# Kernel optimization log

Measured on AMD Instinct MI355X. Metric: run time of the kernel, lower is better.

The kernel has to match this reference:

```python
import jax, jax.numpy as jnp
import numpy as np

N_NODES = 10000
N_EDGES = 320000
DIM = 256
NUM_HEADS = 8
HEAD_DIM = DIM // NUM_HEADS


def setup_inputs() -> dict:
    key = jax.random.key(0)
    ks = jax.random.split(key, 8)
    s = 1.0 / np.sqrt(DIM)
    x = jax.random.normal(ks[0], (N_NODES, DIM), dtype=jnp.float32)
    src = jax.random.randint(ks[1], (N_EDGES,), 0, N_NODES, dtype=jnp.int32)
    dst = jax.random.randint(ks[2], (N_EDGES,), 0, N_NODES, dtype=jnp.int32)
    Wq = jax.random.normal(ks[3], (DIM, DIM), dtype=jnp.float32) * s
    Wk = jax.random.normal(ks[4], (DIM, DIM), dtype=jnp.float32) * s
    Wv = jax.random.normal(ks[5], (DIM, DIM), dtype=jnp.float32) * s
    Wo = jax.random.normal(ks[6], (DIM, DIM), dtype=jnp.float32) * s
    z = jnp.zeros((DIM,), dtype=jnp.float32)
    return {"x": x, "src": src, "dst": dst,
            "Wq": Wq, "bq": z, "Wk": Wk, "bk": z,
            "Wv": Wv, "bv": z, "Wo": Wo, "bo": z}


def reference(x, src, dst, Wq, bq, Wk, bk, Wv, bv, Wo, bo):
    N = x.shape[0]
    # nn.Linear: y = x @ W.T + b
    q = (x @ Wq.T + bq).reshape(N, NUM_HEADS, HEAD_DIM)
    k = (x @ Wk.T + bk).reshape(N, NUM_HEADS, HEAD_DIM)
    v = (x @ Wv.T + bv).reshape(N, NUM_HEADS, HEAD_DIM)
    # u_dot_v: dot(q[src], k[dst]) per head -> [E, H]
    score = jnp.einsum('ehd,ehd->eh', q[src], k[dst]) / np.sqrt(HEAD_DIM).astype(np.float32)
    # Faithful to source: F.softmax(dim=1) on [E, H, 1] -> softmax over HEADS axis
    attn = jax.nn.softmax(score, axis=1)  # [E, H]
    # u_mul_e then sum-reduce onto destination nodes
    m = v[src] * attn[:, :, None]  # [E, H, HEAD_DIM]
    h = jax.ops.segment_sum(m, dst, num_segments=N).reshape(N, DIM)
    out = h @ Wo.T + bo
    # dropout p=0.0 -> identity
    return out
```

## Files before the change

### kernel.cpp

```cpp
#include <hip/hip_runtime.h>
#include <stdint.h>

#define N_NODES 10000
#define N_EDGES 320000
#define DIM 256
#define NRANGE 4
#define RANGE_DIV 2500
#define PAD_SLOTS 32

typedef _Float16 half8 __attribute__((ext_vector_type(8)));
typedef _Float16 half2t __attribute__((ext_vector_type(2)));
typedef float floatx4 __attribute__((ext_vector_type(4)));

#define QK_SCALE 0.17677669529663687f

typedef __attribute__((address_space(3))) uint32_t lds_u32;
typedef __attribute__((address_space(1))) const uint32_t glob_u32;
__device__ __forceinline__ void load16_lds(const _Float16* g, _Float16* l) {
  __builtin_amdgcn_global_load_lds((glob_u32*)g, (lds_u32*)l, 16, 0, 0);
}

__device__ __forceinline__ half8 cvt8s(const float4 a, const float4 b, float sc) {
  half8 o;
  o[0] = (_Float16)(a.x * sc); o[1] = (_Float16)(a.y * sc);
  o[2] = (_Float16)(a.z * sc); o[3] = (_Float16)(a.w * sc);
  o[4] = (_Float16)(b.x * sc); o[5] = (_Float16)(b.y * sc);
  o[6] = (_Float16)(b.z * sc); o[7] = (_Float16)(b.w * sc);
  return o;
}

__global__ void __launch_bounds__(256) prep_k(
    const float* __restrict__ x, const float* __restrict__ Wq,
    const float* __restrict__ Wk, const float* __restrict__ Wv,
    const float* __restrict__ Wo,
    _Float16* __restrict__ xh, _Float16* __restrict__ Wcat,
    _Float16* __restrict__ Woh) {
  int b = blockIdx.x;
  int t = threadIdx.x;
  if (b < 1250) {
    int i = b * 256 + t;
    const float4* p = (const float4*)x;
    ((half8*)xh)[i] = cvt8s(p[2 * i], p[2 * i + 1], 1.0f);
  } else {
    int bb = b - 1250;
    int w = bb >> 5;
    int i = (bb & 31) * 256 + t;
    const float* in = (w == 0) ? Wq : (w == 1) ? Wv : (w == 2) ? Wk : Wo;
    _Float16* out = (w < 3) ? (Wcat + (size_t)w * 65536) : Woh;
    float sc = (w == 0) ? QK_SCALE : 1.0f;
    const float4* p = (const float4*)in;
    ((half8*)out)[i] = cvt8s(p[2 * i], p[2 * i + 1], sc);
  }
}

template <int MODE>
__global__ void __launch_bounds__(256) gemm_tiled(
    const _Float16* __restrict__ A, const _Float16* __restrict__ B,
    const float* __restrict__ b0, const float* __restrict__ b1,
    const float* __restrict__ b2,
    _Float16* __restrict__ qv, _Float16* __restrict__ kh,
    float* __restrict__ outf, int M) {
  __shared__ _Float16 As[8192];
  __shared__ _Float16 Bs[8192];
  int t = threadIdx.x;
  int lane = t & 63;
  int wid = t >> 6;
  int l16 = lane & 15;
  int quad = lane >> 4;
  int wm = wid >> 1, wn = wid & 1;
  int m0 = blockIdx.x * 128;
  int n0 = blockIdx.y * 128;

  floatx4 acc[4][4];
#pragma unroll
  for (int i = 0; i < 4; ++i)
#pragma unroll
    for (int j = 0; j < 4; ++j) acc[i][j] = (floatx4){0.f, 0.f, 0.f, 0.f};

  for (int ks = 0; ks < 4; ++ks) {
    if (ks) __syncthreads();
#pragma unroll
    for (int i = 0; i < 4; ++i) {
      int idx = i * 4 + wid;
      int c = idx >> 1;
      int h = idx & 1;
      int r = h * 64 + lane;
      int ar = m0 + r;
      if (ar >= M) ar = M - 1;
      load16_lds(A + (size_t)ar * 256 + ks * 64 + c * 8, &As[(c * 128 + h * 64) * 8]);
      load16_lds(B + (size_t)(n0 + r) * 256 + ks * 64 + c * 8, &Bs[(c * 128 + h * 64) * 8]);
    }
    __syncthreads();
#pragma unroll
    for (int kk = 0; kk < 2; ++kk) {
      int j = kk * 4 + quad;
      half8 af[4], bf[4];
#pragma unroll
      for (int i = 0; i < 4; ++i) {
        af[i] = *(const half8*)&As[(j * 128 + wm * 64 + i * 16 + l16) * 8];
        bf[i] = *(const half8*)&Bs[(j * 128 + wn * 64 + i * 16 + l16) * 8];
      }
#pragma unroll
      for (int mi = 0; mi < 4; ++mi)
#pragma unroll
        for (int ni = 0; ni < 4; ++ni)
          acc[mi][ni] =
              __builtin_amdgcn_mfma_f32_16x16x32_f16(af[mi], bf[ni], acc[mi][ni], 0, 0, 0);
    }
  }

#pragma unroll
  for (int mi = 0; mi < 4; ++mi) {
#pragma unroll
    for (int ni = 0; ni < 4; ++ni) {
      int col = n0 + wn * 64 + ni * 16 + l16;
      float bias;
      if (MODE == 0) {
        bias = (col < 256) ? b0[col] * QK_SCALE
                           : (col < 512) ? b1[col - 256] : b2[col - 512];
      } else {
        bias = b0[col];
      }
#pragma unroll
      for (int r = 0; r < 4; ++r) {
        int row = m0 + wm * 64 + mi * 16 + quad * 4 + r;
        if (row < M) {
          float val = acc[mi][ni][r] + bias;
          if (MODE == 0) {
            if (col < 512)
              qv[(size_t)row * 512 + col] = (_Float16)val;
            else
              kh[(size_t)row * 256 + (col - 512)] = (_Float16)val;
          } else {
            outf[(size_t)row * 256 + col] = val;
          }
        }
      }
    }
  }
}

__global__ void scatter_k(const int* __restrict__ dst, const int* __restrict__ src,
                          int* __restrict__ cnt4, int* __restrict__ slist4) {
  int e = blockIdx.x * blockDim.x + threadIdx.x;
  if (e < N_EDGES) {
    int s = src[e];
    int r = s / RANGE_DIV;
    int cell = dst[e] * NRANGE + r;
    int pos = atomicAdd(&cnt4[cell], 1);
    if (pos < PAD_SLOTS) slist4[cell * PAD_SLOTS + pos] = s;
  }
}

__global__ void __launch_bounds__(256) aggregate_k(
    const _Float16* __restrict__ qv, const _Float16* __restrict__ kh,
    const int* __restrict__ slist4, const int* __restrict__ cnt4,
    _Float16* __restrict__ hh) {
  int lane = threadIdx.x & 63;
  int n = blockIdx.x * 4 + (threadIdx.x >> 6);
  if (n >= N_NODES) return;
  int h = lane & 7;
  int g = lane >> 3;

  half8 kc[4];
  const half8* krow = (const half8*)(kh + (size_t)n * DIM + h * 32);
#pragma unroll
  for (int i = 0; i < 4; ++i) kc[i] = krow[i];
  const half2t* k2 = (const half2t*)kc;

  half2t acc[16];
#pragma unroll
  for (int i = 0; i < 16; ++i) acc[i] = (half2t){(_Float16)0.f, (_Float16)0.f};

#pragma unroll 1
  for (int r = 0; r < NRANGE; ++r) {
    int cell = n * NRANGE + r;
    int deg = cnt4[cell];
    if (deg > PAD_SLOTS) deg = PAD_SLOTS;
    if (deg == 0) continue;
    const int* base = slist4 + (size_t)cell * PAD_SLOTS;
    int sid = 0;
    if (lane < deg) sid = base[lane];
    int iters = (deg + 7) >> 3;

    int idx = g;
    int s = __shfl(sid, idx);
    const half8* rr = (const half8*)(qv + (size_t)s * 512 + h * 32);
    half8 qc[4], vc[4];
#pragma unroll
    for (int i = 0; i < 4; ++i) { qc[i] = rr[i]; vc[i] = rr[32 + i]; }
    bool valid = idx < deg;

    for (int jj = 0; jj < iters; ++jj) {
      half8 nq[4], nv[4];
      bool nvalid = false;
      if (jj + 1 < iters) {
        int nidx = (jj + 1) * 8 + g;
        int ns = __shfl(sid, nidx);
        const half8* nr = (const half8*)(qv + (size_t)ns * 512 + h * 32);
#pragma unroll
        for (int i = 0; i < 4; ++i) { nq[i] = nr[i]; nv[i] = nr[32 + i]; }
        nvalid = nidx < deg;
      }
      const half2t* q2 = (const half2t*)qc;
      float pa = 0.f, pb = 0.f, pc = 0.f, pd = 0.f;
#pragma unroll
      for (int i = 0; i < 4; ++i) {
#if __has_builtin(__builtin_amdgcn_fdot2)
        pa = __builtin_amdgcn_fdot2(q2[i], k2[i], pa, false);
        pb = __builtin_amdgcn_fdot2(q2[4 + i], k2[4 + i], pb, false);
        pc = __builtin_amdgcn_fdot2(q2[8 + i], k2[8 + i], pc, false);
        pd = __builtin_amdgcn_fdot2(q2[12 + i], k2[12 + i], pd, false);
#else
        pa += (float)q2[i][0] * (float)k2[i][0] + (float)q2[i][1] * (float)k2[i][1];
        pb += (float)q2[4 + i][0] * (float)k2[4 + i][0] + (float)q2[4 + i][1] * (float)k2[4 + i][1];
        pc += (float)q2[8 + i][0] * (float)k2[8 + i][0] + (float)q2[8 + i][1] * (float)k2[8 + i][1];
        pd += (float)q2[12 + i][0] * (float)k2[12 + i][0] + (float)q2[12 + i][1] * (float)k2[12 + i][1];
#endif
      }
      float p = (pa + pb) + (pc + pd);
      float ex = __expf(p);
      float ssum = ex;
      ssum += __shfl_xor(ssum, 1);
      ssum += __shfl_xor(ssum, 2);
      ssum += __shfl_xor(ssum, 4);
      float a = valid ? (ex * __frcp_rn(ssum)) : 0.f;
      _Float16 ah = (_Float16)a;
      half2t ah2 = (half2t){ah, ah};
      const half2t* v2 = (const half2t*)vc;
#pragma unroll
      for (int i = 0; i < 16; ++i) acc[i] += v2[i] * ah2;
#pragma unroll
      for (int i = 0; i < 4; ++i) { qc[i] = nq[i]; vc[i] = nv[i]; }
      valid = nvalid;
    }
  }

#pragma unroll
  for (int i = 0; i < 16; ++i) {
    union { half2t h2; int v; } u;
    u.h2 = acc[i]; u.v = __shfl_xor(u.v, 8);  acc[i] += u.h2;
    u.h2 = acc[i]; u.v = __shfl_xor(u.v, 16); acc[i] += u.h2;
    u.h2 = acc[i]; u.v = __shfl_xor(u.v, 32); acc[i] += u.h2;
  }
  if (g == 0) {
    half8* hrow = (half8*)(hh + (size_t)n * DIM + h * 32);
    const half8* a8 = (const half8*)acc;
#pragma unroll
    for (int i = 0; i < 4; ++i) hrow[i] = a8[i];
  }
}

extern "C" void kernel_launch(void* const* d_in, const int* in_sizes, int n_in,
                              void* d_out, int out_size, void* d_ws, size_t ws_size,
                              hipStream_t stream) {
  const float* x = (const float*)d_in[0];
  const int* src = (const int*)d_in[1];
  const int* dst = (const int*)d_in[2];
  const float* Wq = (const float*)d_in[3];
  const float* bq = (const float*)d_in[4];
  const float* Wk = (const float*)d_in[5];
  const float* bk = (const float*)d_in[6];
  const float* Wv = (const float*)d_in[7];
  const float* bv = (const float*)d_in[8];
  const float* Wo = (const float*)d_in[9];
  const float* bo = (const float*)d_in[10];

  char* p = (char*)d_ws;
  const size_t SZ_NODE_H = (size_t)N_NODES * DIM * sizeof(_Float16);
  _Float16* xh = (_Float16*)p; p += SZ_NODE_H;
  _Float16* qvv = (_Float16*)p; p += 2 * SZ_NODE_H;
  _Float16* kh = (_Float16*)p; p += SZ_NODE_H;
  _Float16* hh = (_Float16*)p; p += SZ_NODE_H;
  _Float16* Wcat = (_Float16*)p; p += (size_t)768 * 256 * sizeof(_Float16);
  _Float16* Woh = (_Float16*)p; p += (size_t)256 * 256 * sizeof(_Float16);
  int* cnt4 = (int*)p; p += (size_t)N_NODES * NRANGE * sizeof(int);
  int* slist4 = (int*)p; p += (size_t)N_NODES * NRANGE * PAD_SLOTS * sizeof(int);

  hipMemsetAsync(cnt4, 0, (size_t)N_NODES * NRANGE * sizeof(int), stream);

  prep_k<<<1378, 256, 0, stream>>>(x, Wq, Wk, Wv, Wo, xh, Wcat, Woh);

  gemm_tiled<0><<<dim3(79, 6), 256, 0, stream>>>(xh, Wcat, bq, bv, bk, qvv, kh,
                                                 nullptr, N_NODES);

  scatter_k<<<(N_EDGES + 255) / 256, 256, 0, stream>>>(dst, src, cnt4, slist4);

  aggregate_k<<<2500, 256, 0, stream>>>(qvv, kh, slist4, cnt4, hh);

  gemm_tiled<1><<<dim3(79, 2), 256, 0, stream>>>(hh, Woh, bo, nullptr, nullptr,
                                                 nullptr, nullptr, (float*)d_out,
                                                 N_NODES);
}
```

Measured before the change: 178.3 us.

## Fuse edge scatter into prep kernel and double-buffer GEMM LDS tiles

Moves the edge-bucketing scatter into the prep kernel as extra blocks, which removes one kernel launch and lets the atomic scatter run concurrently with the fp16 conversion. The tiled GEMM now double-buffers its A/B LDS tiles, prefetching the next k-slice with global_load_lds while MFMAs run on the current one. This doubles LDS use per block to 64KB, which may reduce occupancy. Correctness relies on global_load_lds completing before the end-of-iteration barrier.

```diff
diff --git a/kernel.cpp b/kernel.cpp
--- a/kernel.cpp
+++ b/kernel.cpp
@@ -32,16 +32,18 @@
 __global__ void __launch_bounds__(256) prep_k(
     const float* __restrict__ x, const float* __restrict__ Wq,
     const float* __restrict__ Wk, const float* __restrict__ Wv,
-    const float* __restrict__ Wo,
+    const float* __restrict__ Wo, const int* __restrict__ src,
+    const int* __restrict__ dst,
     _Float16* __restrict__ xh, _Float16* __restrict__ Wcat,
-    _Float16* __restrict__ Woh) {
+    _Float16* __restrict__ Woh, int* __restrict__ cnt4,
+    int* __restrict__ slist4) {
   int b = blockIdx.x;
   int t = threadIdx.x;
   if (b < 1250) {
     int i = b * 256 + t;
     const float4* p = (const float4*)x;
     ((half8*)xh)[i] = cvt8s(p[2 * i], p[2 * i + 1], 1.0f);
-  } else {
+  } else if (b < 1378) {
     int bb = b - 1250;
     int w = bb >> 5;
     int i = (bb & 31) * 256 + t;
@@ -50,6 +52,13 @@
     float sc = (w == 0) ? QK_SCALE : 1.0f;
     const float4* p = (const float4*)in;
     ((half8*)out)[i] = cvt8s(p[2 * i], p[2 * i + 1], sc);
+  } else {
+    int e = (b - 1378) * 256 + t;
+    int s = src[e];
+    int r = s / RANGE_DIV;
+    int cell = dst[e] * NRANGE + r;
+    int pos = atomicAdd(&cnt4[cell], 1);
+    if (pos < PAD_SLOTS) slist4[cell * PAD_SLOTS + pos] = s;
   }
 }
 
@@ -60,8 +69,8 @@
     const float* __restrict__ b2,
     _Float16* __restrict__ qv, _Float16* __restrict__ kh,
     float* __restrict__ outf, int M) {
-  __shared__ _Float16 As[8192];
-  __shared__ _Float16 Bs[8192];
+  __shared__ _Float16 As[16384];
+  __shared__ _Float16 Bs[16384];
   int t = threadIdx.x;
   int lane = t & 63;
   int wid = t >> 6;
@@ -77,8 +86,7 @@
 #pragma unroll
     for (int j = 0; j < 4; ++j) acc[i][j] = (floatx4){0.f, 0.f, 0.f, 0.f};
 
-  for (int ks = 0; ks < 4; ++ks) {
-    if (ks) __syncthreads();
+  auto stage = [&](int ks, int buf) {
 #pragma unroll
     for (int i = 0; i < 4; ++i) {
       int idx = i * 4 + wid;
@@ -87,18 +95,27 @@
       int r = h * 64 + lane;
       int ar = m0 + r;
       if (ar >= M) ar = M - 1;
-      load16_lds(A + (size_t)ar * 256 + ks * 64 + c * 8, &As[(c * 128 + h * 64) * 8]);
-      load16_lds(B + (size_t)(n0 + r) * 256 + ks * 64 + c * 8, &Bs[(c * 128 + h * 64) * 8]);
-    }
-    __syncthreads();
+      load16_lds(A + (size_t)ar * 256 + ks * 64 + c * 8,
+                 &As[buf * 8192 + (c * 128 + h * 64) * 8]);
+      load16_lds(B + (size_t)(n0 + r) * 256 + ks * 64 + c * 8,
+                 &Bs[buf * 8192 + (c * 128 + h * 64) * 8]);
+    }
+  };
+
+  stage(0, 0);
+  __syncthreads();
+
+  for (int ks = 0; ks < 4; ++ks) {
+    int bsel = ks & 1;
+    if (ks < 3) stage(ks + 1, 1 - bsel);
 #pragma unroll
     for (int kk = 0; kk < 2; ++kk) {
       int j = kk * 4 + quad;
       half8 af[4], bf[4];
 #pragma unroll
       for (int i = 0; i < 4; ++i) {
-        af[i] = *(const half8*)&As[(j * 128 + wm * 64 + i * 16 + l16) * 8];
-        bf[i] = *(const half8*)&Bs[(j * 128 + wn * 64 + i * 16 + l16) * 8];
+        af[i] = *(const half8*)&As[bsel * 8192 + (j * 128 + wm * 64 + i * 16 + l16) * 8];
+        bf[i] = *(const half8*)&Bs[bsel * 8192 + (j * 128 + wn * 64 + i * 16 + l16) * 8];
       }
 #pragma unroll
       for (int mi = 0; mi < 4; ++mi)
@@ -107,6 +124,7 @@
           acc[mi][ni] =
               __builtin_amdgcn_mfma_f32_16x16x32_f16(af[mi], bf[ni], acc[mi][ni], 0, 0, 0);
     }
+    __syncthreads();
   }
 
 #pragma unroll
@@ -137,18 +155,6 @@
         }
       }
     }
-  }
-}
-
-__global__ void scatter_k(const int* __restrict__ dst, const int* __restrict__ src,
-                          int* __restrict__ cnt4, int* __restrict__ slist4) {
-  int e = blockIdx.x * blockDim.x + threadIdx.x;
-  if (e < N_EDGES) {
-    int s = src[e];
-    int r = s / RANGE_DIV;
-    int cell = dst[e] * NRANGE + r;
-    int pos = atomicAdd(&cnt4[cell], 1);
-    if (pos < PAD_SLOTS) slist4[cell * PAD_SLOTS + pos] = s;
   }
 }
 
@@ -279,12 +285,11 @@
 
   hipMemsetAsync(cnt4, 0, (size_t)N_NODES * NRANGE * sizeof(int), stream);
 
-  prep_k<<<1378, 256, 0, stream>>>(x, Wq, Wk, Wv, Wo, xh, Wcat, Woh);
+  prep_k<<<2628, 256, 0, stream>>>(x, Wq, Wk, Wv, Wo, src, dst, xh, Wcat, Woh,
+                                   cnt4, slist4);
 
   gemm_tiled<0><<<dim3(79, 6), 256, 0, stream>>>(xh, Wcat, bq, bv, bk, qvv, kh,
                                                  nullptr, N_NODES);
-
-  scatter_k<<<(N_EDGES + 255) / 256, 256, 0, stream>>>(dst, src, cnt4, slist4);
 
   aggregate_k<<<2500, 256, 0, stream>>>(qvv, kh, slist4, cnt4, hh);
 
```

New measurement: 176.1 us. No clear change (-1.2%).
